# Kernel tuning notes

Hardware: AMD Instinct MI355X
Metric: run time of the kernel (lower is better)

Reference implementation:

```python
import jax, jax.numpy as jnp
import numpy as np
from jax import lax

GROUPS = 8            # _resolve_groups(256, 8) == 8
EPS = 1e-5            # GroupNorm default eps
TOPK_RATIO = 0.2
MEAN_W, TOPK_W = 0.7, 0.3
DMG_THRESH = 0.5
DN = ('NCHW', 'OIHW', 'NCHW')


def _normalize(p, axis=1):
    # clamp_min(1e-8) / clamp_min(1e-8).sum().clamp_min(1e-8)
    p = jnp.maximum(p, 1e-8)
    return p / jnp.maximum(p.sum(axis=axis, keepdims=True), 1e-8)


def _conv_head(x, w1, gn_s, gn_b, w2, b2):
    # Conv3x3(no bias) -> GroupNorm(8) -> GELU(exact) -> Dropout(eval: identity) -> Conv1x1
    h = lax.conv_general_dilated(x, w1, (1, 1), 'SAME', dimension_numbers=DN)
    B, C, H, W = h.shape
    hg = h.reshape(B, GROUPS, C // GROUPS, H, W)
    mu = jnp.mean(hg, axis=(2, 3, 4), keepdims=True)
    var = jnp.var(hg, axis=(2, 3, 4), keepdims=True)
    h = ((hg - mu) * lax.rsqrt(var + EPS)).reshape(B, C, H, W)
    h = h * gn_s[None, :, None, None] + gn_b[None, :, None, None]
    h = jax.nn.gelu(h, approximate=False)
    return lax.conv_general_dilated(h, w2, (1, 1), 'SAME', dimension_numbers=DN) + b2[None, :, None, None]


def _forward(feature_map, target_mask, dw1, dgs, dgb, dw2, db2, sw1, sgs, sgb, sw2, sb2):
    dmg_logit = _conv_head(feature_map, dw1, dgs, dgb, dw2, db2)      # [B,1,H,W]
    corn_logits = _conv_head(feature_map, sw1, sgs, sgb, sw2, sb2)    # [B,2,H,W]

    # CORN dense decode: threshold probs = cumprod(sigmoid), classes = K+1
    t = jnp.cumprod(jax.nn.sigmoid(corn_logits), axis=1)              # [B,2,H,W]
    sev = jnp.concatenate([1.0 - t[:, :1], t[:, :-1] - t[:, 1:], t[:, -1:]], axis=1)  # [B,3,H,W]
    sev = _normalize(sev, axis=1)

    p_dmg = jax.nn.sigmoid(dmg_logit)                                 # [B,1,H,W]
    pix = jnp.concatenate([1.0 - p_dmg, p_dmg * sev], axis=1)         # [B,4,H,W]
    pix = _normalize(pix, axis=1)

    sev_pred = jnp.argmax(sev, axis=1) + 1                            # [B,H,W]
    pred_labels = jnp.where(p_dmg[:, 0] >= DMG_THRESH, sev_pred, 0)

    # target_mask already at feature resolution -> nearest resize is identity
    valid = target_mask > 0.5                                         # [B,1,H,W] bool
    B, C, H, W = pix.shape
    N = H * W
    flat = pix.transpose(0, 2, 3, 1).reshape(B, N, C)                 # [B,N,C]
    mf = valid.reshape(B, N)                                          # [B,N]
    cnt = mf.sum(axis=1)                                              # [B] int
    uniform = jnp.full((B, C), 1.0 / C, dtype=flat.dtype)

    # masked mean
    denom = jnp.maximum(cnt, 1).astype(flat.dtype)[:, None]
    mean_p = (flat * mf[..., None]).sum(axis=1) / denom
    mean_p = jnp.where((cnt == 0)[:, None], uniform, mean_p)
    mean_p = _normalize(mean_p, axis=1)

    # masked top-k mean via descending sort + cumsum gather (probs >= 0, invalid -> -1)
    masked = jnp.where(mf[..., None], flat, jnp.asarray(-1.0, flat.dtype))
    srt = -jnp.sort(-masked, axis=1)                                  # descending [B,N,C]
    csum = jnp.cumsum(srt, axis=1)
    k = jnp.clip(jnp.round(cnt.astype(jnp.float32) * TOPK_RATIO).astype(jnp.int32), 1, jnp.maximum(cnt, 1))
    idx = jnp.broadcast_to((k - 1)[:, None, None], (B, 1, C))
    topk_p = jnp.take_along_axis(csum, idx, axis=1)[:, 0] / k.astype(flat.dtype)[:, None]
    topk_p = jnp.where((cnt == 0)[:, None], uniform, topk_p)
    topk_p = _normalize(topk_p, axis=1)

    agg = _normalize(MEAN_W * mean_p + TOPK_W * topk_p, axis=1)
    agg_labels = jnp.argmax(agg, axis=1)

    return (dmg_logit, corn_logits, pix, pred_labels, mean_p, topk_p, agg, agg_labels)


def setup_inputs() -> dict:
    key = jax.random.key(0)
    ks = jax.random.split(key, 8)
    B, Cin, Ch, H, W = 8, 256, 256, 128, 128
    inp = {
        'feature_map': jax.random.normal(ks[0], (B, Cin, H, W), jnp.float32),
        'target_mask': jax.random.uniform(ks[1], (B, 1, H, W), jnp.float32),
        # damage head: Conv3x3 -> GN -> Conv1x1 (1 out)
        'dw1': jax.random.normal(ks[2], (Ch, Cin, 3, 3), jnp.float32) * 0.05,
        'dgs': jnp.ones((Ch,), jnp.float32),
        'dgb': jnp.zeros((Ch,), jnp.float32),
        'dw2': jax.random.normal(ks[3], (1, Ch, 1, 1), jnp.float32) * 0.05,
        'db2': jnp.zeros((1,), jnp.float32),
        # severity head: Conv3x3 -> GN -> Conv1x1 (2 thresholds)
        'sw1': jax.random.normal(ks[4], (Ch, Cin, 3, 3), jnp.float32) * 0.05,
        'sgs': jnp.ones((Ch,), jnp.float32),
        'sgb': jnp.zeros((Ch,), jnp.float32),
        'sw2': jax.random.normal(ks[5], (2, Ch, 1, 1), jnp.float32) * 0.05,
        'sb2': jnp.zeros((2,), jnp.float32),
    }
    return inp


def reference(feature_map, target_mask, dw1, dgs, dgb, dw2, db2, sw1, sgs, sgb, sw2, sb2):
    return _forward(feature_map, target_mask, dw1, dgs, dgb, dw2, db2, sw1, sgs, sgb, sw2, sb2)
```

## Files before the change

### kernel.cpp

```cpp
#include <hip/hip_runtime.h>
#include <hip/hip_bf16.h>

#define BB   8
#define CIN  256
#define CHN  256
#define HH   128
#define WWD  128
#define HW   (HH * WWD)
#define GRP_ELEMS ((size_t)32 * HW)

#define FLAG_DL   4e-3f
#define FLAG_GAP  1.5e-3f

#define BO_DSUM1   0
#define BO_DSUM2   1024
#define BO_FSTAT1  2048
#define BO_FSTAT2  2560
#define BO_DSTAT1  3072
#define BO_DSTAT2  4096
#define BO_MEAN    5120
#define BO_CNT     5248
#define BO_TOPK    5280
#define BO_FLAGC   5408
#define MEMSET_BYTES 8192
#define BO_WL      8192
#define WLCAP      32768

#define XP_OFF    139264ull
#define XP_BYTES  67108864ull
#define HB_OFF    (XP_OFF + XP_BYTES)
#define HB_BYTES  134217728ull
#define WH_OFF    (HB_OFF + HB_BYTES)
#define WT1_ELEMS 589824
#define WH2_BYTES 2359296ull
#define WL2_OFF   (WH_OFF + WH2_BYTES)
#define WT32_OFF  (WL2_OFF + WH2_BYTES)
#define WT32_BYTES 4718592ull
#define HB2_OFF   (WT32_OFF + WT32_BYTES)
#define NEED_B    (WT32_OFF + WT32_BYTES)
#define NEED_A    (HB2_OFF + HB_BYTES)

#define O_DMG   0
#define O_CORN  131072
#define O_PIX   393216
#define O_LAB   917504
#define O_MEAN  1048576
#define O_TOPK  1048608
#define O_AGG   1048640
#define O_ALAB  1048672

typedef __attribute__((ext_vector_type(8))) _Float16 f16x8;
typedef __attribute__((ext_vector_type(4))) float f32x4;

__device__ inline ushort f2h(float f) {
    _Float16 h = (_Float16)f;
    union { _Float16 h; ushort u; } c; c.h = h; return c.u;
}
__device__ inline float h2f(ushort u) {
    union { ushort u; _Float16 h; } c; c.u = u; return (float)c.h;
}

__device__ inline void store4v(float* p, float a, float b, float c, float d) {
    *(float4*)p = make_float4(a, b, c, d);
}
__device__ inline void store4v(__hip_bfloat16* p, float a, float b, float c, float d) {
    p[0] = __float2bfloat16(a); p[1] = __float2bfloat16(b);
    p[2] = __float2bfloat16(c); p[3] = __float2bfloat16(d);
}
__device__ inline float ldv(const float* p) { return *p; }
__device__ inline float ldv(const __hip_bfloat16* p) { return __bfloat162float(*p); }


__global__ __launch_bounds__(256) void pack_x_f16(
    const float* __restrict__ x, ushort* __restrict__ Xh)
{
    int bid = blockIdx.x;
    int cc = bid & 7;
    int y  = (bid >> 3) & 127;
    int b  = bid >> 10;
    __shared__ ushort tile[32][137];
    const int tid = threadIdx.x;
    for (int i = tid; i < 1024; i += 256) {
        int ci = i >> 5;
        int x4 = (i & 31) << 2;
        float4 v = *(const float4*)&x[(((size_t)b * 256 + cc * 32 + ci) * 128 + y) * 128 + x4];
        tile[ci][x4 + 0] = f2h(v.x);
        tile[ci][x4 + 1] = f2h(v.y);
        tile[ci][x4 + 2] = f2h(v.z);
        tile[ci][x4 + 3] = f2h(v.w);
    }
    __syncthreads();
    ushort* dst = Xh + ((((size_t)b * 128 + y) * 8 + cc) << 12);
    for (int i = tid; i < 512; i += 256) {
        int xx  = i >> 2;
        int ci0 = (i & 3) << 3;
        ushort tmp[8];
#pragma unroll
        for (int j = 0; j < 8; j++) tmp[j] = tile[ci0 + j][xx];
        *(uint4*)&dst[i << 3] = *(uint4*)tmp;
    }
}

__global__ __launch_bounds__(256) void transpose_w(
    const float* __restrict__ w, ushort* __restrict__ Whh,
    ushort* __restrict__ Whl, float* __restrict__ Wt32)
{
    __shared__ float lt[8][33];
    int idx = blockIdx.x * 256 + threadIdx.x;
    int tap = idx >> 16;
    int rem = idx & 65535;
    int cc  = rem >> 13;
    int co  = (rem >> 5) & 255;
    int ci5 = rem & 31;
    int ci  = cc * 32 + ci5;
    float v = w[((size_t)co * 256 + ci) * 9 + tap];
    ushort h = f2h(v);
    int sidx = (((tap * 8 + cc) * 16 + (co >> 4)) << 9)
             + (((co & 15) + ((ci5 >> 3) << 4)) << 3) + (ci5 & 7);
    Whh[sidx] = h;
    Whl[sidx] = f2h(v - h2f(h));
    lt[threadIdx.x >> 5][ci5] = v;
    __syncthreads();
    int co_base = (blockIdx.x * 8) & 255;
    int ci5w = threadIdx.x >> 3;
    int j    = threadIdx.x & 7;
    Wt32[((size_t)tap * 256 + cc * 32 + ci5w) * 256 + co_base + j] = lt[j][ci5w];
}

__device__ __forceinline__ void gld16(const void* g, void* l)
{
    __builtin_amdgcn_global_load_lds(
        (const __attribute__((address_space(1))) void*)g,
        (__attribute__((address_space(3))) void*)l, 16, 0, 0);
}

__device__ __forceinline__ void issue_b_slice(
    const ushort* __restrict__ Whh, const ushort* __restrict__ Whl,
    ushort* dst, int u, int co0, int tid, int wb)
{
    const int su  = u / 3;
    const int kxu = u - su * 3;
    const int tap = ((su >> 3) * 3) + kxu;
    const int cc  = su & 7;
    const size_t sbase = ((size_t)((tap * 8 + cc) * 16 + (co0 >> 4)) << 9);
    const ushort* s0 = Whh + sbase;
    const ushort* s1 = Whl + sbase;
#pragma unroll
    for (int k = 0; k < 2; k++)
        gld16(s0 + (k * 256 + tid) * 8, dst + (size_t)(k * 256 + wb) * 8);
#pragma unroll
    for (int k = 0; k < 2; k++)
        gld16(s1 + (k * 256 + tid) * 8, dst + 4096 + (size_t)(k * 256 + wb) * 8);
}

__device__ __forceinline__ void issue_a_slice(
    const ushort* __restrict__ Xh, const ushort* __restrict__ zb,
    ushort* dst, int b, int y, int sn, int tid, int wb)
{
    const int kyn = sn >> 3, ccn = sn & 7;
    const int rown = y + kyn - 1;
    const bool rv = (unsigned)rown < 128u;
    const ushort* base = rv ? (Xh + ((((size_t)b * 128 + rown) * 8 + ccn) << 12)) : zb;
#pragma unroll
    for (int k = 0; k < 2; k++) {
        int idx = k * 256 + tid;
        int xi  = (idx + 4) >> 2;
        int q   = (idx & 3) ^ ((xi >> 1) & 3);
        int off = rv ? ((xi - 1) * 32 + q * 8) : (idx * 8);
        gld16(base + off, dst + 32 + (size_t)(k * 256 + wb) * 8);
    }
}

template <int MERGED>
__global__ __launch_bounds__(256, 3) void conv3x3_mfma(
    const ushort* __restrict__ Xh, const ushort* __restrict__ Whh,
    const ushort* __restrict__ Whl, const ushort* __restrict__ zb,
    float* __restrict__ hb1, float* __restrict__ hb2,
    double* __restrict__ sums, int headfix)
{
    __shared__ ushort a_lds[2][4160];
    __shared__ ushort b_lds[2][8192];
    __shared__ float sred[8];

    const int bxr = blockIdx.x;
    const int y   = bxr >> 3;
    const int b   = bxr & 7;
    const int by  = blockIdx.y;
    const int head = MERGED ? (by >> 1) : headfix;
    const int co0  = MERGED ? ((by & 1) << 7) : (by << 7);
    const ushort* WhhH = Whh + head * WT1_ELEMS;
    const ushort* WhlH = Whl + head * WT1_ELEMS;
    float* hout = head ? hb2 : hb1;
    double* sumsH = sums + head * 128;

    const int tid  = threadIdx.x;
    const int lane = tid & 63;
    const int wb   = tid & 192;
    const int wv   = tid >> 6;
    const int m = lane & 15;
    const int q = lane >> 4;
    const int wpx = (wv & 1) << 6;
    const int wco = (wv >> 1) << 6;
    const int g0  = wco >> 4;

    if (tid < 8) sred[tid] = 0.f;
    if (tid < 16) {
        int tg = tid >> 2, p4 = tid & 3;
        ushort* r = &a_lds[tg >> 1][(tg & 1) ? (129 * 32) : 0];
        *(uint4*)(r + p4 * 8) = make_uint4(0u, 0u, 0u, 0u);
    }

    f32x4 acc[4][4];
#pragma unroll
    for (int f = 0; f < 4; f++)
#pragma unroll
        for (int g = 0; g < 4; g++) acc[f][g] = (f32x4){0.f, 0.f, 0.f, 0.f};

    issue_a_slice(Xh, zb, a_lds[0], b, y, 0, tid, wb);
    issue_b_slice(WhhH, WhlH, b_lds[0], 0, co0, tid, wb);
    asm volatile("s_waitcnt lgkmcnt(0)" ::: "memory");

    for (int s = 0; s < 24; s++) {
        const ushort* acur = a_lds[s & 1];
#pragma unroll
        for (int kx = 0; kx < 3; kx++) {
            const int t = 3 * s + kx;
            asm volatile("" ::: "memory");
            __builtin_amdgcn_s_barrier();
            {
                int u = t + 1;
                int ub = u & 1;
                if (u > 71) u = 71;
                issue_b_slice(WhhH, WhlH, b_lds[ub], u, co0, tid, wb);
            }
            if (kx == 0) {
                int sn = s + 1;
                int ab = sn & 1;
                if (sn > 23) sn = 23;
                issue_a_slice(Xh, zb, a_lds[ab], b, y, sn, tid, wb);
            }
            if (kx == 2) asm volatile("s_waitcnt vmcnt(4)" ::: "memory");
            else         asm volatile("s_waitcnt vmcnt(6)" ::: "memory");
            __builtin_amdgcn_s_barrier();
            asm volatile("" ::: "memory");

            const ushort* bb = b_lds[t & 1];
            f16x8 ah[4], bh[4], bl[4];
#pragma unroll
            for (int f = 0; f < 4; f++) {
                int row = wpx + f * 16 + kx + m;
                ah[f] = *(const f16x8*)(acur + row * 32
                        + ((q ^ ((row >> 1) & 3)) << 3));
            }
#pragma unroll
            for (int g = 0; g < 4; g++) {
                int off = ((g0 + g) << 9) + (lane << 3);
                bh[g] = *(const f16x8*)&bb[off];
                bl[g] = *(const f16x8*)&bb[4096 + off];
            }
            __builtin_amdgcn_s_setprio(1);
#pragma unroll
            for (int f = 0; f < 4; f++)
#pragma unroll
                for (int g = 0; g < 4; g++)
                    acc[f][g] = __builtin_amdgcn_mfma_f32_16x16x32_f16(ah[f], bh[g], acc[f][g], 0, 0, 0);
#pragma unroll
            for (int f = 0; f < 4; f++)
#pragma unroll
                for (int g = 0; g < 4; g++)
                    acc[f][g] = __builtin_amdgcn_mfma_f32_16x16x32_f16(ah[f], bl[g], acc[f][g], 0, 0, 0);
            __builtin_amdgcn_s_setprio(0);
        }
    }

    float s0 = 0.f, q0 = 0.f, s1 = 0.f, q1 = 0.f;
#pragma unroll
    for (int f = 0; f < 4; f++) {
#pragma unroll
        for (int g = 0; g < 4; g++) {
            f32x4 v = acc[f][g];
            float a = v.x + v.y + v.z + v.w;
            float qq = v.x * v.x + v.y * v.y + v.z * v.z + v.w * v.w;
            if (g < 2) { s0 += a; q0 += qq; } else { s1 += a; q1 += qq; }
            int px = wpx + f * 16 + q * 4;
            int co = co0 + wco + g * 16 + m;
            *(f32x4*)&hout[((size_t)(b * 256 + co) * 128 + y) * 128 + px] = v;
        }
    }
    int gl = wco >> 5;
    atomicAdd(&sred[gl],     s0);
    atomicAdd(&sred[gl + 1], s1);
    atomicAdd(&sred[4 + gl],     q0);
    atomicAdd(&sred[4 + gl + 1], q1);
    __syncthreads();
    if (tid < 4) atomicAdd(&sumsH[b * 8 + (co0 >> 5) + tid], (double)sred[tid]);
    else if (tid < 8) atomicAdd(&sumsH[64 + b * 8 + (co0 >> 5) + tid - 4], (double)sred[tid]);
}

template <typename HT>
__global__ __launch_bounds__(256) void conv3x3_gn_stats(
    const float* __restrict__ x, const float* __restrict__ w,
    HT* __restrict__ hout, double* __restrict__ sums)
{
    __shared__ float in_lds[8][3][132];
    __shared__ float w_lds[8][9][68];
    __shared__ float sred[2], qred[2];

    const int bx  = blockIdx.x;
    const int y   = bx & (HH - 1);
    const int b   = bx >> 7;
    const int co0 = blockIdx.y << 6;
    const int tid = threadIdx.x;
    if (tid < 2) { sred[tid] = 0.f; qred[tid] = 0.f; }
    const int tco = (tid & 15) << 2;
    const int tox = (tid >> 4) << 3;

    float acc[4][8];
#pragma unroll
    for (int i = 0; i < 4; i++)
#pragma unroll
        for (int j = 0; j < 8; j++) acc[i][j] = 0.f;

    const float* xb = x + (size_t)b * CIN * HW;
    for (int c0 = 0; c0 < CIN; c0 += 8) {
        __syncthreads();
        for (int i = tid; i < 8 * 3 * 130; i += 256) {
            int ci  = i / 390;
            int rem = i - ci * 390;
            int r   = rem / 130;
            int cx  = rem - r * 130;
            int gy  = y + r - 1;
            int gx  = cx - 1;
            float v = 0.f;
            if ((unsigned)gy < HH && (unsigned)gx < WWD)
                v = xb[(size_t)(c0 + ci) * HW + gy * WWD + gx];
            in_lds[ci][r][cx] = v;
        }
        for (int i = tid; i < 64 * 72; i += 256) {
            int co = i / 72;
            int kk = i - co * 72;
            int ci = kk / 9;
            int k9 = kk - ci * 9;
            w_lds[ci][k9][co] = w[((size_t)(co0 + co) * CIN + (c0 + ci)) * 9 + k9];
        }
        __syncthreads();
#pragma unroll
        for (int ci = 0; ci < 8; ci++) {
#pragma unroll
            for (int ky = 0; ky < 3; ky++) {
                const float* rowp = &in_lds[ci][ky][tox];
                float4 a0 = *(const float4*)rowp;
                float4 a1 = *(const float4*)(rowp + 4);
                float2 a2 = *(const float2*)(rowp + 8);
                float in10[10] = {a0.x, a0.y, a0.z, a0.w,
                                  a1.x, a1.y, a1.z, a1.w, a2.x, a2.y};
#pragma unroll
                for (int kx = 0; kx < 3; kx++) {
                    float4 wv = *(const float4*)&w_lds[ci][ky * 3 + kx][tco];
#pragma unroll
                    for (int ox = 0; ox < 8; ox++) {
                        float iv = in10[ox + kx];
                        acc[0][ox] = fmaf(iv, wv.x, acc[0][ox]);
                        acc[1][ox] = fmaf(iv, wv.y, acc[1][ox]);
                        acc[2][ox] = fmaf(iv, wv.z, acc[2][ox]);
                        acc[3][ox] = fmaf(iv, wv.w, acc[3][ox]);
                    }
                }
            }
        }
// ... 13 lines not shown
    const int gsel = tco >> 5;
    atomicAdd(&sred[gsel], s);
    atomicAdd(&qred[gsel], qv);
    __syncthreads();
    if (tid < 2) {
        int grp = (co0 >> 5) + tid;
        atomicAdd(&sums[b * 8 + grp],      (double)sred[tid]);
        atomicAdd(&sums[64 + b * 8 + grp], (double)qred[tid]);
    }
}

__global__ void gn_finalize(const double* __restrict__ dsums,
                            float* __restrict__ fstats, double* __restrict__ dstats)
{
    int i = threadIdx.x;
    if (i < 64) {
        double inv = 1.0 / (double)GRP_ELEMS;
        double mu  = dsums[i] * inv;
        double ex2 = dsums[64 + i] * inv;
        double var = ex2 - mu * mu;
        double rs  = 1.0 / sqrt(var + 1e-5);
        fstats[i]      = (float)mu;
        fstats[64 + i] = (float)rs;
        dstats[i]      = mu;
        dstats[64 + i] = rs;
    }
}

__global__ void gn_finalize_all(const double* __restrict__ dsums,
                                float* __restrict__ fstats, double* __restrict__ dstats)
{
    int i = threadIdx.x;
    if (i < 128) {
        int head = i >> 6, j = i & 63;
        double inv = 1.0 / (double)GRP_ELEMS;
        double mu  = dsums[head * 128 + j] * inv;
        double ex2 = dsums[head * 128 + 64 + j] * inv;
        double var = ex2 - mu * mu;
        double rs  = 1.0 / sqrt(var + 1e-5);
        fstats[head * 128 + j]      = (float)mu;
        fstats[head * 128 + 64 + j] = (float)rs;
        dstats[head * 128 + j]      = mu;
        dstats[head * 128 + 64 + j] = rs;
    }
}

template <typename HT>
__global__ __launch_bounds__(256) void gn_head(
    const HT* __restrict__ hbuf,
    const float* __restrict__ gs, const float* __restrict__ gb,
    const float* __restrict__ w2, const float* __restrict__ b2,
    const float* __restrict__ stats,
    float* __restrict__ out, int nout)
{
    __shared__ float sc[256], sh[256], w2s[2][256];
    const int b = blockIdx.y;
    const int p = blockIdx.x * 256 + threadIdx.x;
    {
        int c = threadIdx.x;
        float mu = stats[b * 8 + (c >> 5)];
        float rs = stats[64 + b * 8 + (c >> 5)];
        float s  = gs[c] * rs;
        sc[c] = s;
        sh[c] = gb[c] - mu * s;
        w2s[0][c] = w2[c];
        w2s[1][c] = (nout > 1) ? w2[256 + c] : 0.f;
    }
    __syncthreads();
    const HT* hp = hbuf + (size_t)b * CHN * HW + p;
    float a0 = 0.f, a1 = 0.f;
#pragma unroll 16
    for (int c = 0; c < 256; c++) {
        float v = ldv(hp + (size_t)c * HW);
        v = fmaf(v, sc[c], sh[c]);
        float g = 0.5f * v * (1.f + erff(v * 0.70710678118654752440f));
        a0 = fmaf(g, w2s[0][c], a0);
        a1 = fmaf(g, w2s[1][c], a1);
    }
    out[(size_t)b * nout * HW + p] = a0 + b2[0];
    if (nout > 1) out[(size_t)b * nout * HW + HW + p] = a1 + b2[1];
}

__global__ __launch_bounds__(256) void gn_head_m(
    const float* __restrict__ hb1, const float* __restrict__ hb2,
    const float* __restrict__ dgs, const float* __restrict__ dgb,
    const float* __restrict__ dw2, const float* __restrict__ db2,
    const float* __restrict__ sgs, const float* __restrict__ sgb,
    const float* __restrict__ sw2, const float* __restrict__ sb2,
    const float* __restrict__ fstats, float* __restrict__ out)
{
    __shared__ float sc[256], sh[256], w2s[2][256];
    const int head = blockIdx.z;
    const float* hbuf = head ? hb2 : hb1;
    const float* gs = head ? sgs : dgs;
    const float* gb = head ? sgb : dgb;
    const float* w2 = head ? sw2 : dw2;
    const float* b2 = head ? sb2 : db2;
    const float* stats = fstats + head * 128;
    const int b = blockIdx.y;
    const int p = blockIdx.x * 256 + threadIdx.x;
    {
        int c = threadIdx.x;
        float mu = stats[b * 8 + (c >> 5)];
        float rs = stats[64 + b * 8 + (c >> 5)];
        float s  = gs[c] * rs;
        sc[c] = s;
        sh[c] = gb[c] - mu * s;
        w2s[0][c] = w2[c];
        w2s[1][c] = head ? w2[256 + c] : 0.f;
    }
    __syncthreads();
    const float* hp = hbuf + (size_t)b * CHN * HW + p;
    float a0 = 0.f, a1 = 0.f;
#pragma unroll 16
    for (int c = 0; c < 256; c++) {
        float v = hp[(size_t)c * HW];
        v = fmaf(v, sc[c], sh[c]);
        float g = 0.5f * v * (1.f + erff(v * 0.70710678118654752440f));
        a0 = fmaf(g, w2s[0][c], a0);
        a1 = fmaf(g, w2s[1][c], a1);
    }
    if (head == 0) {
        out[O_DMG + (size_t)b * HW + p] = a0 + b2[0];
    } else {
        out[O_CORN + (size_t)b * 2 * HW + p]      = a0 + b2[0];
        out[O_CORN + (size_t)b * 2 * HW + HW + p] = a1 + b2[1];
    }
}

__global__ __launch_bounds__(256) void decode_kernel(
    float* __restrict__ outw, const float* __restrict__ mask,
    float* __restrict__ meanacc, float* __restrict__ cntacc,
    int* __restrict__ flagcnt, int* __restrict__ wl)
{
    const int b = blockIdx.y;
    const int p = blockIdx.x * 256 + threadIdx.x;

    float dl = outw[O_DMG + b * HW + p];
    float c0 = outw[O_CORN + (b * 2 + 0) * HW + p];
    float c1 = outw[O_CORN + (b * 2 + 1) * HW + p];

    float s0 = 1.f / (1.f + expf(-c0));
    float s1 = 1.f / (1.f + expf(-c1));
    float t0 = s0, t1 = s0 * s1;
    float e0 = fmaxf(1.f - t0, 1e-8f);
    float e1 = fmaxf(t0 - t1, 1e-8f);
    float e2 = fmaxf(t1, 1e-8f);
    float es = fmaxf(e0 + e1 + e2, 1e-8f);
    e0 /= es; e1 /= es; e2 /= es;

    float pd = 1.f / (1.f + expf(-dl));
    float q0 = fmaxf(1.f - pd, 1e-8f);
    float q1 = fmaxf(pd * e0, 1e-8f);
    float q2 = fmaxf(pd * e1, 1e-8f);
    float q3 = fmaxf(pd * e2, 1e-8f);
    float qs = fmaxf(q0 + q1 + q2 + q3, 1e-8f);
    q0 /= qs; q1 /= qs; q2 /= qs; q3 /= qs;

    outw[O_PIX + ((size_t)b * 4 + 0) * HW + p] = q0;
    outw[O_PIX + ((size_t)b * 4 + 1) * HW + p] = q1;
    outw[O_PIX + ((size_t)b * 4 + 2) * HW + p] = q2;
    outw[O_PIX + ((size_t)b * 4 + 3) * HW + p] = q3;

    int am = 0; float bv = e0;
    if (e1 > bv) { bv = e1; am = 1; }
    if (e2 > bv) { bv = e2; am = 2; }
    outw[O_LAB + b * HW + p] = (pd >= 0.5f) ? (float)(am + 1) : 0.f;

    bool flag = (fabsf(dl) < FLAG_DL);
    {
        float top1 = e0, top2 = fmaxf(e1, e2);
        if (e1 > top1) { top1 = e1; top2 = fmaxf(e0, e2); }
        if (e2 > top1) { top1 = e2; top2 = fmaxf(e0, e1); }
        if ((top1 - top2 < FLAG_GAP) && (dl > -FLAG_DL)) flag = true;
    }
    if (flag) {
        int idx = atomicAdd(flagcnt, 1);
        if (idx < WLCAP) wl[idx] = b * HW + p;
    }

    bool valid = mask[b * HW + p] > 0.5f;
    float vm = valid ? 1.f : 0.f;
    float v0 = valid ? q0 : 0.f, v1 = valid ? q1 : 0.f;
    float v2 = valid ? q2 : 0.f, v3 = valid ? q3 : 0.f;

#pragma unroll
    for (int o = 32; o; o >>= 1) {
        v0 += __shfl_down(v0, o); v1 += __shfl_down(v1, o);
        v2 += __shfl_down(v2, o); v3 += __shfl_down(v3, o);
        vm += __shfl_down(vm, o);
    }
    __shared__ float racc[5];
    if (threadIdx.x < 5) racc[threadIdx.x] = 0.f;
    __syncthreads();
    if ((threadIdx.x & 63) == 0) {
        atomicAdd(&racc[0], v0); atomicAdd(&racc[1], v1);
        atomicAdd(&racc[2], v2); atomicAdd(&racc[3], v3);
        atomicAdd(&racc[4], vm);
    }
    __syncthreads();
    if (threadIdx.x < 4) atomicAdd(&meanacc[b * 4 + threadIdx.x], racc[threadIdx.x]);
    if (threadIdx.x == 4) atomicAdd(&cntacc[b], racc[4]);
}

__global__ __launch_bounds__(256) void fixup_labels(
    const float* __restrict__ x, const float* __restrict__ Wt32,
    const float* __restrict__ dgs, const float* __restrict__ dgb,
    const float* __restrict__ dw2, const float* __restrict__ db2,
    const float* __restrict__ sgs, const float* __restrict__ sgb,
    const float* __restrict__ sw2, const float* __restrict__ sb2,
    const double* __restrict__ dstat1, const double* __restrict__ dstat2,
    const int* __restrict__ wl, const int* __restrict__ wcnt,
    float* __restrict__ out)
{
    __shared__ float xp[2304];
    __shared__ double dpart[4][256];
    __shared__ double wred[3][4];

    int count = *wcnt;
    if (count > WLCAP) count = WLCAP;
    const int tid  = threadIdx.x;
    const int lane = tid & 63;
    const int wv   = tid >> 6;
    const int c4   = lane << 2;
    const int j0   = wv * 576;

    for (int pix = blockIdx.x; pix < count; pix += gridDim.x) {
        __syncthreads();
        const int pid = wl[pix];
        const int b = pid >> 14, yy = (pid >> 7) & 127, xx = pid & 127;
        for (int i = tid; i < 2304; i += 256) {
            int t = i >> 8, ci = i & 255;
            int ky = t / 3, kx = t - ky * 3;
            int gy = yy + ky - 1, gx = xx + kx - 1;
            float v = 0.f;
            if ((unsigned)gy < 128u && (unsigned)gx < 128u)
                v = x[(((size_t)b * 256 + ci) * 128 + gy) * 128 + gx];
            xp[i] = v;
        }
        __syncthreads();

        for (int head = 0; head < 2; head++) {
            const float* gs  = head ? sgs : dgs;
            const float* gb  = head ? sgb : dgb;
            const float* w2  = head ? sw2 : dw2;
            const double* st = head ? dstat2 : dstat1;
            const float* wt  = Wt32 + (size_t)head * 589824;

            double a0 = 0.0, a1 = 0.0, a2 = 0.0, a3 = 0.0;
            for (int jc = 0; jc < 576; jc += 8) {
                float4 wv4[8];
#pragma unroll
                for (int u = 0; u < 8; u++)
                    wv4[u] = *(const float4*)&wt[(size_t)(j0 + jc + u) * 256 + c4];
#pragma unroll
                for (int u = 0; u < 8; u++) {
                    double xv = (double)xp[j0 + jc + u];
                    a0 += xv * (double)wv4[u].x;
                    a1 += xv * (double)wv4[u].y;
                    a2 += xv * (double)wv4[u].z;
                    a3 += xv * (double)wv4[u].w;
                }
            }
            dpart[wv][c4]     = a0;
            dpart[wv][c4 + 1] = a1;
            dpart[wv][c4 + 2] = a2;
            dpart[wv][c4 + 3] = a3;
            __syncthreads();

            {
                const int c = tid;
                double h = dpart[0][c] + dpart[1][c] + dpart[2][c] + dpart[3][c];
                double mu = st[b * 8 + (c >> 5)];
                double rs = st[64 + b * 8 + (c >> 5)];
                double v = (h - mu) * rs * (double)gs[c] + (double)gb[c];
                double g = 0.5 * v * (1.0 + erf(v * 0.70710678118654752440));
                double r0 = g * (double)w2[c];
#pragma unroll
                for (int o = 32; o; o >>= 1) r0 += __shfl_down(r0, o);
                if (lane == 0) wred[head][wv] = r0;
                if (head == 1) {
                    double r1 = g * (double)w2[256 + c];
#pragma unroll
                    for (int o = 32; o; o >>= 1) r1 += __shfl_down(r1, o);
                    if (lane == 0) wred[2][wv] = r1;
                }
            }
            __syncthreads();
        }

        if (tid == 0) {
            double dlv = wred[0][0] + wred[0][1] + wred[0][2] + wred[0][3] + (double)db2[0];
            double c0v = wred[1][0] + wred[1][1] + wred[1][2] + wred[1][3] + (double)sb2[0];
            double c1v = wred[2][0] + wred[2][1] + wred[2][2] + wred[2][3] + (double)sb2[1];
            double s0 = 1.0 / (1.0 + exp(-c0v));
            double s1 = 1.0 / (1.0 + exp(-c1v));
            double t0 = s0, t1 = s0 * s1;
            double e0 = fmax(1.0 - t0, 1e-8);
            double e1 = fmax(t0 - t1, 1e-8);
            double e2 = fmax(t1, 1e-8);
            int am = 0; double bv = e0;
            if (e1 > bv) { bv = e1; am = 1; }
            if (e2 > bv) { bv = e2; am = 2; }
            out[O_LAB + pid] = (dlv >= 0.0) ? (float)(am + 1) : 0.f;
        }
    }
}

__global__ __launch_bounds__(256) void topk_kernel(
    const float* __restrict__ outw, const float* __restrict__ mask,
    const float* __restrict__ cntacc, float* __restrict__ topkout)
{
    const int b = blockIdx.x >> 2;
    const int c = blockIdx.x & 3;
    const int tid = threadIdx.x;

    __shared__ int hist[256];
    __shared__ unsigned s_prefix;
    __shared__ int s_want;
    __shared__ float s_red[4];
    __shared__ int s_redi[4];

    float cntf = cntacc[b];
    int cnt = (int)cntf;
    int k = (int)rintf(cntf * 0.2f);
    if (k < 1) k = 1;
    int kmax = cnt > 1 ? cnt : 1;
    if (k > kmax) k = kmax;

    if (tid == 0) { s_prefix = 0u; s_want = k; }

    const float* pv = outw + O_PIX + ((size_t)b * 4 + c) * HW;
    const float* pm = mask + (size_t)b * HW;

    unsigned uv[64];
#pragma unroll
    for (int j = 0; j < 64; j++) {
        int p = tid + (j << 8);
        float v = (pm[p] > 0.5f) ? pv[p] : -1.0f;
        unsigned bits = __float_as_uint(v);
        uv[j] = (bits & 0x80000000u) ? ~bits : (bits | 0x80000000u);
    }

    for (int pass = 0; pass < 4; pass++) {
        hist[tid] = 0;
        __syncthreads();
        const int shift = 24 - 8 * pass;
        const unsigned pmask = pass ? (0xFFFFFFFFu << (shift + 8)) : 0u;
        const unsigned prefix = s_prefix;
#pragma unroll
        for (int j = 0; j < 64; j++) {
            unsigned u = uv[j];
            if ((u & pmask) == prefix) atomicAdd(&hist[(u >> shift) & 255], 1);
        }
        __syncthreads();
        if (tid == 0) {
            int want = s_want;
            int bin = 255;
            while (bin > 0) {
                int h = hist[bin];
                if (want <= h) break;
                want -= h;
                bin--;
            }
            s_want = want;
            s_prefix = prefix | ((unsigned)bin << shift);
        }
        __syncthreads();
    }
    const unsigned tau = s_prefix;

    float sgt = 0.f; int cgt = 0;
#pragma unroll
    for (int j = 0; j < 64; j++) {
        unsigned u = uv[j];
        if (u > tau) {
            unsigned bits = (u & 0x80000000u) ? (u & 0x7FFFFFFFu) : ~u;
// ... 13 lines not shown
        float total = S + (float)(k - C) * tf;
        topkout[b * 4 + c] = total / (float)k;
    }
}

__device__ inline void norm4(float* p)
{
    float a = fmaxf(p[0], 1e-8f), b = fmaxf(p[1], 1e-8f);
    float c = fmaxf(p[2], 1e-8f), d = fmaxf(p[3], 1e-8f);
    float s = fmaxf(a + b + c + d, 1e-8f);
    p[0] = a / s; p[1] = b / s; p[2] = c / s; p[3] = d / s;
}

__global__ void final_kernel(const float* __restrict__ meanacc,
                             const float* __restrict__ cntacc,
                             const float* __restrict__ topkv,
                             float* __restrict__ outw)
{
    int b = threadIdx.x;
    if (b >= 8) return;
    float cnt = cntacc[b];
    bool zero = (cnt == 0.f);
    float denom = fmaxf(cnt, 1.f);
    float m[4], t[4], a[4];
#pragma unroll
    for (int c = 0; c < 4; c++) {
        m[c] = zero ? 0.25f : meanacc[b * 4 + c] / denom;
        t[c] = zero ? 0.25f : topkv[b * 4 + c];
    }
    norm4(m); norm4(t);
#pragma unroll
    for (int c = 0; c < 4; c++) a[c] = 0.7f * m[c] + 0.3f * t[c];
    norm4(a);
    int am = 0; float bv = a[0];
#pragma unroll
    for (int c = 1; c < 4; c++) if (a[c] > bv) { bv = a[c]; am = c; }
#pragma unroll
    for (int c = 0; c < 4; c++) {
        outw[O_MEAN + b * 4 + c] = m[c];
        outw[O_TOPK + b * 4 + c] = t[c];
        outw[O_AGG  + b * 4 + c] = a[c];
    }
    outw[O_ALAB + b] = (float)am;
}

extern "C" void kernel_launch(void* const* d_in, const int* in_sizes, int n_in,
                              void* d_out, int out_size, void* d_ws, size_t ws_size,
                              hipStream_t stream)
{
    (void)in_sizes; (void)n_in; (void)out_size;
    const float* x    = (const float*)d_in[0];
    const float* mask = (const float*)d_in[1];
    const float* dw1  = (const float*)d_in[2];
    const float* dgs  = (const float*)d_in[3];
    const float* dgb  = (const float*)d_in[4];
    const float* dw2  = (const float*)d_in[5];
    const float* db2  = (const float*)d_in[6];
    const float* sw1  = (const float*)d_in[7];
    const float* sgs  = (const float*)d_in[8];
    const float* sgb  = (const float*)d_in[9];
    const float* sw2  = (const float*)d_in[10];
    const float* sb2  = (const float*)d_in[11];
    float* out = (float*)d_out;

    char* wsb = (char*)d_ws;
    double* dsum1  = (double*)(wsb + BO_DSUM1);
    double* dsum2  = (double*)(wsb + BO_DSUM2);
    float*  fstat1 = (float*)(wsb + BO_FSTAT1);
    float*  fstat2 = (float*)(wsb + BO_FSTAT2);
    double* dstat1 = (double*)(wsb + BO_DSTAT1);
    double* dstat2 = (double*)(wsb + BO_DSTAT2);
    float*  meanacc = (float*)(wsb + BO_MEAN);
    float*  cntacc  = (float*)(wsb + BO_CNT);
    float*  topkv   = (float*)(wsb + BO_TOPK);
    int*    flagc   = (int*)(wsb + BO_FLAGC);
    int*    wl      = (int*)(wsb + BO_WL);

    hipMemsetAsync(d_ws, 0, MEMSET_BYTES + 8192, stream);

    dim3 pgrid(64, BB);

    if (ws_size >= NEED_B) {
        ushort* Xh   = (ushort*)(wsb + XP_OFF);
        float*  hb1  = (float*)(wsb + HB_OFF);
        ushort* Whh  = (ushort*)(wsb + WH_OFF);
        ushort* Whl  = (ushort*)(wsb + WL2_OFF);
        float*  Wt32 = (float*)(wsb + WT32_OFF);
        const ushort* zb = (const ushort*)(wsb + BO_WL);

        pack_x_f16<<<8192, 256, 0, stream>>>(x, Xh);
        transpose_w<<<2304, 256, 0, stream>>>(dw1, Whh, Whl, Wt32);
        transpose_w<<<2304, 256, 0, stream>>>(sw1, Whh + WT1_ELEMS, Whl + WT1_ELEMS,
                                              Wt32 + WT1_ELEMS);

        if (ws_size >= NEED_A) {
            float* hb2 = (float*)(wsb + HB2_OFF);
            conv3x3_mfma<1><<<dim3(1024, 4), 256, 0, stream>>>(
                Xh, Whh, Whl, zb, hb1, hb2, dsum1, 0);
            gn_finalize_all<<<1, 128, 0, stream>>>(dsum1, fstat1, dstat1);
            gn_head_m<<<dim3(64, BB, 2), 256, 0, stream>>>(
                hb1, hb2, dgs, dgb, dw2, db2, sgs, sgb, sw2, sb2, fstat1, out);
        } else {
            conv3x3_mfma<0><<<dim3(1024, 2), 256, 0, stream>>>(
                Xh, Whh, Whl, zb, hb1, hb1, dsum1, 0);
            gn_finalize<<<1, 64, 0, stream>>>(dsum1, fstat1, dstat1);
            gn_head<float><<<pgrid, 256, 0, stream>>>(hb1, dgs, dgb, dw2, db2,
                                                      fstat1, out + O_DMG, 1);
            conv3x3_mfma<0><<<dim3(1024, 2), 256, 0, stream>>>(
                Xh, Whh, Whl, zb, hb1, hb1, dsum1, 1);
            gn_finalize<<<1, 64, 0, stream>>>(dsum2, fstat2, dstat2);
            gn_head<float><<<pgrid, 256, 0, stream>>>(hb1, sgs, sgb, sw2, sb2,
                                                      fstat2, out + O_CORN, 2);
        }

        decode_kernel<<<pgrid, 256, 0, stream>>>(out, mask, meanacc, cntacc, flagc, wl);
        fixup_labels<<<512, 256, 0, stream>>>(x, Wt32, dgs, dgb, dw2, db2,
                                              sgs, sgb, sw2, sb2,
                                              dstat1, dstat2, wl, flagc, out);
        topk_kernel<<<32, 256, 0, stream>>>(out, mask, cntacc, topkv);
        final_kernel<<<1, 64, 0, stream>>>(meanacc, cntacc, topkv, out);
    } else {
        void* hbuf = wsb + XP_OFF;
        dim3 cgrid(HH * BB, CHN / 64);
        const size_t needF32 = XP_OFF + (size_t)BB * CHN * HW * sizeof(float);
        if (ws_size >= needF32) {
            conv3x3_gn_stats<float><<<cgrid, 256, 0, stream>>>(x, dw1, (float*)hbuf, dsum1);
            gn_finalize<<<1, 64, 0, stream>>>(dsum1, fstat1, dstat1);
            gn_head<float><<<pgrid, 256, 0, stream>>>((float*)hbuf, dgs, dgb, dw2, db2,
                                                      fstat1, out + O_DMG, 1);
            conv3x3_gn_stats<float><<<cgrid, 256, 0, stream>>>(x, sw1, (float*)hbuf, dsum2);
            gn_finalize<<<1, 64, 0, stream>>>(dsum2, fstat2, dstat2);
            gn_head<float><<<pgrid, 256, 0, stream>>>((float*)hbuf, sgs, sgb, sw2, sb2,
                                                      fstat2, out + O_CORN, 2);
        } else {
            conv3x3_gn_stats<__hip_bfloat16><<<cgrid, 256, 0, stream>>>(x, dw1, (__hip_bfloat16*)hbuf, dsum1);
            gn_finalize<<<1, 64, 0, stream>>>(dsum1, fstat1, dstat1);
            gn_head<__hip_bfloat16><<<pgrid, 256, 0, stream>>>((__hip_bfloat16*)hbuf, dgs, dgb, dw2, db2,
                                                               fstat1, out + O_DMG, 1);
            conv3x3_gn_stats<__hip_bfloat16><<<cgrid, 256, 0, stream>>>(x, sw1, (__hip_bfloat16*)hbuf, dsum2);
            gn_finalize<<<1, 64, 0, stream>>>(dsum2, fstat2, dstat2);
            gn_head<__hip_bfloat16><<<pgrid, 256, 0, stream>>>((__hip_bfloat16*)hbuf, sgs, sgb, sw2, sb2,
                                                               fstat2, out + O_CORN, 2);
        }
        decode_kernel<<<pgrid, 256, 0, stream>>>(out, mask, meanacc, cntacc, flagc, wl);
        topk_kernel<<<32, 256, 0, stream>>>(out, mask, cntacc, topkv);
        final_kernel<<<1, 64, 0, stream>>>(meanacc, cntacc, topkv, out);
    }
}
```

Before: 1.255 ms.

## Merge both conv heads into one 512-thread block sharing the input row tile

Replaces the merged conv kernel, which launched 4 blocks per output row (2 heads × 2 channel halves), with a single 512-thread block per row. Its 8 waves cover all 256 output channels of both heads, so each input row slice is loaded into LDS once instead of four times. Each wave now computes 128 pixels × 64 channels with split-f16 weights (hi and lo parts). This uses more LDS and more registers per block, limits occupancy to 2 blocks, and cuts the grid to 1024 blocks. The fallback path keeps the old kernel, renamed to take a single head.

```diff
diff --git a/kernel.cpp b/kernel.cpp
--- a/kernel.cpp
+++ b/kernel.cpp
@@ -134,6 +134,159 @@
         (__attribute__((address_space(3))) void*)l, 16, 0, 0);
 }
 
+__device__ __forceinline__ void issue_b8(
+    const ushort* __restrict__ Whh, const ushort* __restrict__ Whl,
+    ushort* dst, int u, int tid, int wb8)
+{
+    const int su  = u / 3;
+    const int kxu = u - su * 3;
+    const int tap = ((su >> 3) * 3) + kxu;
+    const int cc  = su & 7;
+    const size_t sbase = ((size_t)((tap * 8 + cc) * 16)) << 9;
+#pragma unroll
+    for (int h = 0; h < 2; h++) {
+        const ushort* s0 = Whh + h * WT1_ELEMS + sbase;
+        const ushort* s1 = Whl + h * WT1_ELEMS + sbase;
+        ushort* d = dst + h * 16384;
+#pragma unroll
+        for (int c = 0; c < 2; c++) {
+            gld16(s0 + (size_t)(c * 512 + tid) * 8, d + (size_t)(c * 512 + wb8) * 8);
+            gld16(s1 + (size_t)(c * 512 + tid) * 8, d + 8192 + (size_t)(c * 512 + wb8) * 8);
+        }
+    }
+}
+
+__device__ __forceinline__ void issue_a8(
+    const ushort* __restrict__ Xh, const ushort* __restrict__ zb,
+    ushort* dst, int b, int y, int sn, int tid, int wb8)
+{
+    const int kyn = sn >> 3, ccn = sn & 7;
+    const int rown = y + kyn - 1;
+    const bool rv = (unsigned)rown < 128u;
+    const ushort* base = rv ? (Xh + ((((size_t)b * 128 + rown) * 8 + ccn) << 12)) : zb;
+    int xi  = (tid + 4) >> 2;
+    int q   = (tid & 3) ^ ((xi >> 1) & 3);
+    int off = rv ? ((xi - 1) * 32 + q * 8) : (tid * 8);
+    gld16(base + off, dst + 32 + (size_t)wb8 * 8);
+}
+
+__global__ __launch_bounds__(512, 2) void conv3x3_mfma8(
+    const ushort* __restrict__ Xh, const ushort* __restrict__ Whh,
+    const ushort* __restrict__ Whl, const ushort* __restrict__ zb,
+    float* __restrict__ hb1, float* __restrict__ hb2,
+    double* __restrict__ sums)
+{
+    __shared__ ushort a_lds[2][4160];
+    __shared__ ushort b_lds[2][2][16384];
+    __shared__ float sred[32];
+
+    const int bxr = blockIdx.x;
+    const int y   = bxr >> 3;
+    const int b   = bxr & 7;
+    const int tid  = threadIdx.x;
+    const int lane = tid & 63;
+    const int wb8  = tid & 448;
+    const int wv   = tid >> 6;
+    const int head = wv >> 2;
+    const int q4   = wv & 3;
+    const int m = lane & 15;
+    const int q = lane >> 4;
+
+    if (tid < 32) sred[tid] = 0.f;
+    if (tid < 16) {
+        int tg = tid >> 2, p4 = tid & 3;
+        ushort* r = &a_lds[tg >> 1][(tg & 1) ? (129 * 32) : 0];
+        *(uint4*)(r + p4 * 8) = make_uint4(0u, 0u, 0u, 0u);
+    }
+
+    f32x4 acc[8][4];
+#pragma unroll
+    for (int f = 0; f < 8; f++)
+#pragma unroll
+        for (int g = 0; g < 4; g++) acc[f][g] = (f32x4){0.f, 0.f, 0.f, 0.f};
+
+    issue_a8(Xh, zb, a_lds[0], b, y, 0, tid, wb8);
+    issue_b8(Whh, Whl, &b_lds[0][0][0], 0, tid, wb8);
+    asm volatile("s_waitcnt lgkmcnt(0)" ::: "memory");
+
+    for (int s = 0; s < 24; s++) {
+        const ushort* acur = a_lds[s & 1];
+#pragma unroll
+        for (int kx = 0; kx < 3; kx++) {
+            const int t = 3 * s + kx;
+            asm volatile("" ::: "memory");
+            __builtin_amdgcn_s_barrier();
+            {
+                int u = t + 1;
+                int ub = u & 1;
+                if (u > 71) u = 71;
+                issue_b8(Whh, Whl, &b_lds[ub][0][0], u, tid, wb8);
+            }
+            if (kx == 0) {
+                int sn = s + 1;
+                int ab = sn & 1;
+                if (sn > 23) sn = 23;
+                issue_a8(Xh, zb, a_lds[ab], b, y, sn, tid, wb8);
+            }
+            if (kx == 2) asm volatile("s_waitcnt vmcnt(8)" ::: "memory");
+            else         asm volatile("s_waitcnt vmcnt(9)" ::: "memory");
+            __builtin_amdgcn_s_barrier();
+            asm volatile("" ::: "memory");
+
+            const ushort* bbH = &b_lds[t & 1][head][0];
+            f16x8 ah[8];
+#pragma unroll
+            for (int f = 0; f < 8; f++) {
+                int row = f * 16 + kx + m;
+                ah[f] = *(const f16x8*)(acur + row * 32
+                        + ((q ^ ((row >> 1) & 3)) << 3));
+            }
+            __builtin_amdgcn_s_setprio(1);
+#pragma unroll
+            for (int g = 0; g < 4; g++) {
+                int off = ((q4 * 4 + g) << 9) + (lane << 3);
+                f16x8 bh = *(const f16x8*)&bbH[off];
+                f16x8 bl = *(const f16x8*)&bbH[8192 + off];
+#pragma unroll
+                for (int f = 0; f < 8; f++)
+                    acc[f][g] = __builtin_amdgcn_mfma_f32_16x16x32_f16(ah[f], bh, acc[f][g], 0, 0, 0);
+#pragma unroll
+                for (int f = 0; f < 8; f++)
+                    acc[f][g] = __builtin_amdgcn_mfma_f32_16x16x32_f16(ah[f], bl, acc[f][g], 0, 0, 0);
+            }
+            __builtin_amdgcn_s_setprio(0);
+        }
+    }
+
+    float* ho = head ? hb2 : hb1;
+    float s0 = 0.f, q0 = 0.f, s1 = 0.f, q1 = 0.f;
+#pragma unroll
+    for (int f = 0; f < 8; f++) {
+#pragma unroll
+        for (int g = 0; g < 4; g++) {
+            f32x4 v = acc[f][g];
+            float a = v.x + v.y + v.z + v.w;
+            float qq = v.x * v.x + v.y * v.y + v.z * v.z + v.w * v.w;
+            if (g < 2) { s0 += a; q0 += qq; } else { s1 += a; q1 += qq; }
+            int px = f * 16 + q * 4;
+            int co = q4 * 64 + g * 16 + m;
+            *(f32x4*)&ho[((size_t)(b * 256 + co) * 128 + y) * 128 + px] = v;
+        }
+    }
+    int gl = q4 * 2;
+    atomicAdd(&sred[head * 16 + gl],     s0);
+    atomicAdd(&sred[head * 16 + gl + 1], s1);
+    atomicAdd(&sred[head * 16 + 8 + gl],     q0);
+    atomicAdd(&sred[head * 16 + 8 + gl + 1], q1);
+    __syncthreads();
+    if (tid < 32) {
+        int h = tid >> 4, r = tid & 15;
+        if (r < 8) atomicAdd(&sums[h * 128 + b * 8 + r], (double)sred[h * 16 + r]);
+        else       atomicAdd(&sums[h * 128 + 64 + b * 8 + (r - 8)],
+                             (double)sred[h * 16 + r]);
+    }
+}
+
 __device__ __forceinline__ void issue_b_slice(
     const ushort* __restrict__ Whh, const ushort* __restrict__ Whl,
     ushort* dst, int u, int co0, int tid, int wb)
@@ -171,12 +324,10 @@
     }
 }
 
-template <int MERGED>
-__global__ __launch_bounds__(256, 3) void conv3x3_mfma(
+__global__ __launch_bounds__(256, 3) void conv3x3_mfma4(
     const ushort* __restrict__ Xh, const ushort* __restrict__ Whh,
     const ushort* __restrict__ Whl, const ushort* __restrict__ zb,
-    float* __restrict__ hb1, float* __restrict__ hb2,
-    double* __restrict__ sums, int headfix)
+    float* __restrict__ hout, double* __restrict__ sums, int head)
 {
     __shared__ ushort a_lds[2][4160];
     __shared__ ushort b_lds[2][8192];
@@ -185,12 +336,9 @@
     const int bxr = blockIdx.x;
     const int y   = bxr >> 3;
     const int b   = bxr & 7;
-    const int by  = blockIdx.y;
-    const int head = MERGED ? (by >> 1) : headfix;
-    const int co0  = MERGED ? ((by & 1) << 7) : (by << 7);
+    const int co0 = blockIdx.y << 7;
     const ushort* WhhH = Whh + head * WT1_ELEMS;
     const ushort* WhlH = Whl + head * WT1_ELEMS;
-    float* hout = head ? hb2 : hb1;
     double* sumsH = sums + head * 128;
 
     const int tid  = threadIdx.x;
@@ -867,19 +1015,19 @@
 
         if (ws_size >= NEED_A) {
             float* hb2 = (float*)(wsb + HB2_OFF);
-            conv3x3_mfma<1><<<dim3(1024, 4), 256, 0, stream>>>(
-                Xh, Whh, Whl, zb, hb1, hb2, dsum1, 0);
+            conv3x3_mfma8<<<dim3(1024), 512, 0, stream>>>(
+                Xh, Whh, Whl, zb, hb1, hb2, dsum1);
             gn_finalize_all<<<1, 128, 0, stream>>>(dsum1, fstat1, dstat1);
             gn_head_m<<<dim3(64, BB, 2), 256, 0, stream>>>(
                 hb1, hb2, dgs, dgb, dw2, db2, sgs, sgb, sw2, sb2, fstat1, out);
         } else {
-            conv3x3_mfma<0><<<dim3(1024, 2), 256, 0, stream>>>(
-                Xh, Whh, Whl, zb, hb1, hb1, dsum1, 0);
+            conv3x3_mfma4<<<dim3(1024, 2), 256, 0, stream>>>(
+                Xh, Whh, Whl, zb, hb1, dsum1, 0);
             gn_finalize<<<1, 64, 0, stream>>>(dsum1, fstat1, dstat1);
             gn_head<float><<<pgrid, 256, 0, stream>>>(hb1, dgs, dgb, dw2, db2,
                                                       fstat1, out + O_DMG, 1);
-            conv3x3_mfma<0><<<dim3(1024, 2), 256, 0, stream>>>(
-                Xh, Whh, Whl, zb, hb1, hb1, dsum1, 1);
+            conv3x3_mfma4<<<dim3(1024, 2), 256, 0, stream>>>(
+                Xh, Whh, Whl, zb, hb1, dsum1, 1);
             gn_finalize<<<1, 64, 0, stream>>>(dsum2, fstat2, dstat2);
             gn_head<float><<<pgrid, 256, 0, stream>>>(hb1, sgs, sgb, sw2, sb2,
                                                       fstat2, out + O_CORN, 2);
```

Result: no change. 1.269 ms (+1.1%).

## Store conv intermediate in fp16, pack gn_head pixels, batch fixup over pixels

Applied to the files above, without the earlier changes.

The 3x3 conv output buffers become fp16 instead of fp32, which halves the write traffic from the MFMA conv and the read traffic in the GroupNorm/GELU/1x1 head. The head kernel now handles two pixels per thread with 32-bit loads. The fixup kernel, which recomputes flagged pixels in double precision, now processes six pixels per block so each weight load is reused across them. The flag thresholds are widened to catch more borderline pixels, since the fp16 intermediate adds rounding error; this may send more pixels to the fixup path.

```diff
diff --git a/kernel.cpp b/kernel.cpp
--- a/kernel.cpp
+++ b/kernel.cpp
@@ -9,8 +9,8 @@
 #define HW   (HH * WWD)
 #define GRP_ELEMS ((size_t)32 * HW)
 
-#define FLAG_DL   4e-3f
-#define FLAG_GAP  1.5e-3f
+#define FLAG_DL   5e-3f
+#define FLAG_GAP  2e-3f
 
 #define BO_DSUM1   0
 #define BO_DSUM2   1024
@@ -29,7 +29,7 @@
 #define XP_OFF    139264ull
 #define XP_BYTES  67108864ull
 #define HB_OFF    (XP_OFF + XP_BYTES)
-#define HB_BYTES  134217728ull
+#define HB_BYTES  67108864ull
 #define WH_OFF    (HB_OFF + HB_BYTES)
 #define WT1_ELEMS 589824
 #define WH2_BYTES 2359296ull
@@ -67,8 +67,13 @@
     p[0] = __float2bfloat16(a); p[1] = __float2bfloat16(b);
     p[2] = __float2bfloat16(c); p[3] = __float2bfloat16(d);
 }
+__device__ inline void store4v(ushort* p, float a, float b, float c, float d) {
+    ushort t[4] = {f2h(a), f2h(b), f2h(c), f2h(d)};
+    *(uint2*)p = *(uint2*)t;
+}
 __device__ inline float ldv(const float* p) { return *p; }
 __device__ inline float ldv(const __hip_bfloat16* p) { return __bfloat162float(*p); }
+__device__ inline float ldv(const ushort* p) { return h2f(*p); }
 
 
 __global__ __launch_bounds__(256) void pack_x_f16(
@@ -175,7 +180,7 @@
 __global__ __launch_bounds__(256, 3) void conv3x3_mfma(
     const ushort* __restrict__ Xh, const ushort* __restrict__ Whh,
     const ushort* __restrict__ Whl, const ushort* __restrict__ zb,
-    float* __restrict__ hb1, float* __restrict__ hb2,
+    ushort* __restrict__ hb1, ushort* __restrict__ hb2,
     double* __restrict__ sums, int headfix)
 {
     __shared__ ushort a_lds[2][4160];
@@ -190,7 +195,7 @@
     const int co0  = MERGED ? ((by & 1) << 7) : (by << 7);
     const ushort* WhhH = Whh + head * WT1_ELEMS;
     const ushort* WhlH = Whl + head * WT1_ELEMS;
-    float* hout = head ? hb2 : hb1;
+    ushort* hout = head ? hb2 : hb1;
     double* sumsH = sums + head * 128;
 
     const int tid  = threadIdx.x;
@@ -284,7 +289,8 @@
             if (g < 2) { s0 += a; q0 += qq; } else { s1 += a; q1 += qq; }
             int px = wpx + f * 16 + q * 4;
             int co = co0 + wco + g * 16 + m;
-            *(f32x4*)&hout[((size_t)(b * 256 + co) * 128 + y) * 128 + px] = v;
+            store4v(&hout[((size_t)(b * 256 + co) * 128 + y) * 128 + px],
+                    v.x, v.y, v.z, v.w);
         }
     }
     int gl = wco >> 5;
@@ -464,7 +470,7 @@
 }
 
 __global__ __launch_bounds__(256) void gn_head_m(
-    const float* __restrict__ hb1, const float* __restrict__ hb2,
+    const ushort* __restrict__ hb1, const ushort* __restrict__ hb2,
     const float* __restrict__ dgs, const float* __restrict__ dgb,
     const float* __restrict__ dw2, const float* __restrict__ db2,
     const float* __restrict__ sgs, const float* __restrict__ sgb,
@@ -473,14 +479,14 @@
 {
     __shared__ float sc[256], sh[256], w2s[2][256];
     const int head = blockIdx.z;
-    const float* hbuf = head ? hb2 : hb1;
+    const ushort* hbuf = head ? hb2 : hb1;
     const float* gs = head ? sgs : dgs;
     const float* gb = head ? sgb : dgb;
     const float* w2 = head ? sw2 : dw2;
     const float* b2 = head ? sb2 : db2;
     const float* stats = fstats + head * 128;
     const int b = blockIdx.y;
-    const int p = blockIdx.x * 256 + threadIdx.x;
+    const int p = (blockIdx.x * 256 + threadIdx.x) * 2;
     {
         int c = threadIdx.x;
         float mu = stats[b * 8 + (c >> 5)];
@@ -492,21 +498,28 @@
         w2s[1][c] = head ? w2[256 + c] : 0.f;
     }
     __syncthreads();
-    const float* hp = hbuf + (size_t)b * CHN * HW + p;
-    float a0 = 0.f, a1 = 0.f;
-#pragma unroll 16
+    const ushort* hp = hbuf + (size_t)b * CHN * HW + p;
+    float a0 = 0.f, a1 = 0.f, c0 = 0.f, c1 = 0.f;
+#pragma unroll 8
     for (int c = 0; c < 256; c++) {
-        float v = hp[(size_t)c * HW];
-        v = fmaf(v, sc[c], sh[c]);
-        float g = 0.5f * v * (1.f + erff(v * 0.70710678118654752440f));
-        a0 = fmaf(g, w2s[0][c], a0);
-        a1 = fmaf(g, w2s[1][c], a1);
+        uint u = *(const uint*)(hp + (size_t)c * HW);
+        float v0 = fmaf(h2f((ushort)(u & 0xffffu)), sc[c], sh[c]);
+        float v1 = fmaf(h2f((ushort)(u >> 16)),     sc[c], sh[c]);
+        float g0 = 0.5f * v0 * (1.f + erff(v0 * 0.70710678118654752440f));
+        float g1 = 0.5f * v1 * (1.f + erff(v1 * 0.70710678118654752440f));
+        a0 = fmaf(g0, w2s[0][c], a0);
+        c0 = fmaf(g1, w2s[0][c], c0);
+        a1 = fmaf(g0, w2s[1][c], a1);
+        c1 = fmaf(g1, w2s[1][c], c1);
     }
     if (head == 0) {
-        out[O_DMG + (size_t)b * HW + p] = a0 + b2[0];
+        out[O_DMG + (size_t)b * HW + p]     = a0 + b2[0];
+        out[O_DMG + (size_t)b * HW + p + 1] = c0 + b2[0];
     } else {
-        out[O_CORN + (size_t)b * 2 * HW + p]      = a0 + b2[0];
-        out[O_CORN + (size_t)b * 2 * HW + HW + p] = a1 + b2[1];
+        out[O_CORN + (size_t)b * 2 * HW + p]          = a0 + b2[0];
+        out[O_CORN + (size_t)b * 2 * HW + p + 1]      = c0 + b2[0];
+        out[O_CORN + (size_t)b * 2 * HW + HW + p]     = a1 + b2[1];
+        out[O_CORN + (size_t)b * 2 * HW + HW + p + 1] = c1 + b2[1];
     }
 }
 
@@ -585,6 +598,7 @@
     if (threadIdx.x == 4) atomicAdd(&cntacc[b], racc[4]);
 }
 
+#define FIXP 6
 __global__ __launch_bounds__(256) void fixup_labels(
     const float* __restrict__ x, const float* __restrict__ Wt32,
     const float* __restrict__ dgs, const float* __restrict__ dgb,
@@ -595,9 +609,9 @@
     const int* __restrict__ wl, const int* __restrict__ wcnt,
     float* __restrict__ out)
 {
-    __shared__ float xp[2304];
+    __shared__ float xp[FIXP][2304];
     __shared__ double dpart[4][256];
-    __shared__ double wred[3][4];
+    __shared__ double wred[FIXP][3][4];
 
     int count = *wcnt;
     if (count > WLCAP) count = WLCAP;
@@ -607,18 +621,21 @@
     const int c4   = lane << 2;
     const int j0   = wv * 576;
 
-    for (int pix = blockIdx.x; pix < count; pix += gridDim.x) {
+    for (int base = blockIdx.x * FIXP; base < count; base += gridDim.x * FIXP) {
+        int npx = count - base;
+        if (npx > FIXP) npx = FIXP;
         __syncthreads();
-        const int pid = wl[pix];
-        const int b = pid >> 14, yy = (pid >> 7) & 127, xx = pid & 127;
-        for (int i = tid; i < 2304; i += 256) {
-            int t = i >> 8, ci = i & 255;
+        for (int i = tid; i < npx * 2304; i += 256) {
+            int px = i / 2304, j = i - px * 2304;
+            int t = j >> 8, ci = j & 255;
             int ky = t / 3, kx = t - ky * 3;
+            int pid = wl[base + px];
+            int b = pid >> 14, yy = (pid >> 7) & 127, xx = pid & 127;
             int gy = yy + ky - 1, gx = xx + kx - 1;
             float v = 0.f;
             if ((unsigned)gy < 128u && (unsigned)gx < 128u)
                 v = x[(((size_t)b * 256 + ci) * 128 + gy) * 128 + gx];
-            xp[i] = v;
+            xp[px][j] = v;
         }
         __syncthreads();
 
@@ -629,7 +646,12 @@
             const double* st = head ? dstat2 : dstat1;
             const float* wt  = Wt32 + (size_t)head * 589824;
 
-            double a0 = 0.0, a1 = 0.0, a2 = 0.0, a3 = 0.0;
+            double acc[FIXP][4];
+#pragma unroll
+            for (int px = 0; px < FIXP; px++)
+#pragma unroll
+                for (int g = 0; g < 4; g++) acc[px][g] = 0.0;
+
             for (int jc = 0; jc < 576; jc += 8) {
                 float4 wv4[8];
 #pragma unroll
@@ -637,44 +659,58 @@
                     wv4[u] = *(const float4*)&wt[(size_t)(j0 + jc + u) * 256 + c4];
 #pragma unroll
                 for (int u = 0; u < 8; u++) {
-                    double xv = (double)xp[j0 + jc + u];
-                    a0 += xv * (double)wv4[u].x;
-                    a1 += xv * (double)wv4[u].y;
-                    a2 += xv * (double)wv4[u].z;
-                    a3 += xv * (double)wv4[u].w;
+#pragma unroll
+                    for (int px = 0; px < FIXP; px++) {
+                        double xv = (double)xp[px][j0 + jc + u];
+                        acc[px][0] += xv * (double)wv4[u].x;
+                        acc[px][1] += xv * (double)wv4[u].y;
+                        acc[px][2] += xv * (double)wv4[u].z;
+                        acc[px][3] += xv * (double)wv4[u].w;
+                    }
                 }
             }
-            dpart[wv][c4]     = a0;
-            dpart[wv][c4 + 1] = a1;
-            dpart[wv][c4 + 2] = a2;
-            dpart[wv][c4 + 3] = a3;
-            __syncthreads();
-
-            {
-                const int c = tid;
-                double h = dpart[0][c] + dpart[1][c] + dpart[2][c] + dpart[3][c];
-                double mu = st[b * 8 + (c >> 5)];
-                double rs = st[64 + b * 8 + (c >> 5)];
-                double v = (h - mu) * rs * (double)gs[c] + (double)gb[c];
-                double g = 0.5 * v * (1.0 + erf(v * 0.70710678118654752440));
-                double r0 = g * (double)w2[c];
-#pragma unroll
-                for (int o = 32; o; o >>= 1) r0 += __shfl_down(r0, o);
-                if (lane == 0) wred[head][wv] = r0;
-                if (head == 1) {
-                    double r1 = g * (double)w2[256 + c];
-#pragma unroll
-                    for (int o = 32; o; o >>= 1) r1 += __shfl_down(r1, o);
-                    if (lane == 0) wred[2][wv] = r1;
+
+#pragma unroll
+            for (int px = 0; px < FIXP; px++) {
+                if (px < npx) {
+                    dpart[wv][c4]     = acc[px][0];
+                    dpart[wv][c4 + 1] = acc[px][1];
+                    dpart[wv][c4 + 2] = acc[px][2];
+                    dpart[wv][c4 + 3] = acc[px][3];
+                    __syncthreads();
+                    {
+                        const int c = tid;
+                        int pid = wl[base + px];
+                        int b = pid >> 14;
+                        double h = dpart[0][c] + dpart[1][c] + dpart[2][c] + dpart[3][c];
+                        double mu = st[b * 8 + (c >> 5)];
+                        double rs = st[64 + b * 8 + (c >> 5)];
+                        double v = (h - mu) * rs * (double)gs[c] + (double)gb[c];
+                        double g = 0.5 * v * (1.0 + erf(v * 0.70710678118654752440));
+                        double r0 = g * (double)w2[c];
+#pragma unroll
+                        for (int o = 32; o; o >>= 1) r0 += __shfl_down(r0, o);
+                        if (lane == 0) wred[px][head][wv] = r0;
+                        if (head == 1) {
+                            double r1 = g * (double)w2[256 + c];
+#pragma unroll
+                            for (int o = 32; o; o >>= 1) r1 += __shfl_down(r1, o);
+                            if (lane == 0) wred[px][2][wv] = r1;
+                        }
+                    }
+                    __syncthreads();
                 }
             }
-            __syncthreads();
-        }
-
-        if (tid == 0) {
-            double dlv = wred[0][0] + wred[0][1] + wred[0][2] + wred[0][3] + (double)db2[0];
-            double c0v = wred[1][0] + wred[1][1] + wred[1][2] + wred[1][3] + (double)sb2[0];
-            double c1v = wred[2][0] + wred[2][1] + wred[2][2] + wred[2][3] + (double)sb2[1];
+        }
+
+        if (tid < npx) {
+            const int pid = wl[base + tid];
+            double dlv = wred[tid][0][0] + wred[tid][0][1] + wred[tid][0][2]
+                       + wred[tid][0][3] + (double)db2[0];
+            double c0v = wred[tid][1][0] + wred[tid][1][1] + wred[tid][1][2]
+                       + wred[tid][1][3] + (double)sb2[0];
+            double c1v = wred[tid][2][0] + wred[tid][2][1] + wred[tid][2][2]
+                       + wred[tid][2][3] + (double)sb2[1];
             double s0 = 1.0 / (1.0 + exp(-c0v));
             double s1 = 1.0 / (1.0 + exp(-c1v));
             double t0 = s0, t1 = s0 * s1;
@@ -854,7 +890,7 @@
 
     if (ws_size >= NEED_B) {
         ushort* Xh   = (ushort*)(wsb + XP_OFF);
-        float*  hb1  = (float*)(wsb + HB_OFF);
+        ushort* hb1  = (ushort*)(wsb + HB_OFF);
         ushort* Whh  = (ushort*)(wsb + WH_OFF);
         ushort* Whl  = (ushort*)(wsb + WL2_OFF);
         float*  Wt32 = (float*)(wsb + WT32_OFF);
@@ -866,23 +902,23 @@
                                               Wt32 + WT1_ELEMS);
 
         if (ws_size >= NEED_A) {
-            float* hb2 = (float*)(wsb + HB2_OFF);
+            ushort* hb2 = (ushort*)(wsb + HB2_OFF);
             conv3x3_mfma<1><<<dim3(1024, 4), 256, 0, stream>>>(
                 Xh, Whh, Whl, zb, hb1, hb2, dsum1, 0);
             gn_finalize_all<<<1, 128, 0, stream>>>(dsum1, fstat1, dstat1);
-            gn_head_m<<<dim3(64, BB, 2), 256, 0, stream>>>(
+            gn_head_m<<<dim3(32, BB, 2), 256, 0, stream>>>(
                 hb1, hb2, dgs, dgb, dw2, db2, sgs, sgb, sw2, sb2, fstat1, out);
         } else {
             conv3x3_mfma<0><<<dim3(1024, 2), 256, 0, stream>>>(
                 Xh, Whh, Whl, zb, hb1, hb1, dsum1, 0);
             gn_finalize<<<1, 64, 0, stream>>>(dsum1, fstat1, dstat1);
-            gn_head<float><<<pgrid, 256, 0, stream>>>(hb1, dgs, dgb, dw2, db2,
-                                                      fstat1, out + O_DMG, 1);
+            gn_head<ushort><<<pgrid, 256, 0, stream>>>(hb1, dgs, dgb, dw2, db2,
+                                                       fstat1, out + O_DMG, 1);
             conv3x3_mfma<0><<<dim3(1024, 2), 256, 0, stream>>>(
                 Xh, Whh, Whl, zb, hb1, hb1, dsum1, 1);
             gn_finalize<<<1, 64, 0, stream>>>(dsum2, fstat2, dstat2);
-            gn_head<float><<<pgrid, 256, 0, stream>>>(hb1, sgs, sgb, sw2, sb2,
-                                                      fstat2, out + O_CORN, 2);
+            gn_head<ushort><<<pgrid, 256, 0, stream>>>(hb1, sgs, sgb, sw2, sb2,
+                                                       fstat2, out + O_CORN, 2);
         }
 
         decode_kernel<<<pgrid, 256, 0, stream>>>(out, mask, meanacc, cntacc, flagc, wl);
```

Measured after the change: 1.103 ms. -12.1%, faster.
